# Kernel optimization log

Hardware: AMD Instinct MI355X
Metric: run time of the kernel (lower is better)

Reference implementation:

```python
import jax, jax.numpy as jnp
import numpy as np
import math

N_HEAD = 16
N_EMBD = 2048
HEAD_DIM = 128
N_LAYER = 24
EPS = 1e-5


def _get_alibi_slopes(n_heads):
    def pow2(n):
        start = 2 ** (-2 ** (-(math.log2(n) - 3)))
        return [start * start ** i for i in range(n)]
    if math.log2(n_heads).is_integer():
        return pow2(n_heads)
    c = 2 ** math.floor(math.log2(n_heads))
    s = pow2(c)
    extra = _get_alibi_slopes(2 * c)
    return s + extra[0::2][: n_heads - c]

ALIBI_SLOPES = jnp.asarray(np.array(_get_alibi_slopes(N_HEAD), dtype=np.float32))  # (H,)


def rmsnorm(x, w, eps=EPS):
    # fp32 RMSNorm over last dim with affine weight (use_fp32=True path)
    xf = x.astype(jnp.float32)
    out = xf * jax.lax.rsqrt(jnp.mean(xf * xf, axis=-1, keepdims=True) + eps)
    return (out * w.astype(jnp.float32)).astype(x.dtype)


def setup_inputs() -> dict:
    key = jax.random.key(0)
    ks = jax.random.split(key, 8)
    B, T, C, H, D = 2, 2048, N_EMBD, N_HEAD, HEAD_DIM
    sc = 1.0 / math.sqrt(C)
    proj_std = 0.5 / math.sqrt(C) / math.sqrt(N_LAYER)
    return {
        "x": jax.random.normal(ks[0], (B, T, C), jnp.float32),
        "Wq": jax.random.normal(ks[1], (C, H * D), jnp.float32) * sc,
        "Wk": jax.random.normal(ks[2], (C, H * D), jnp.float32) * sc,
        "Wv": jax.random.normal(ks[3], (C, H * D), jnp.float32) * sc,
        "Wproj": jax.random.normal(ks[4], (H * D, C), jnp.float32) * proj_std,
        "q_rms_w": jnp.ones((D,), jnp.float32),
        "k_rms_w": jnp.ones((D,), jnp.float32),
        "subln_w": jnp.ones((D,), jnp.float32),
    }


def reference(x, Wq, Wk, Wv, Wproj, q_rms_w, k_rms_w, subln_w):
    B, T, C = x.shape
    H, D = N_HEAD, HEAD_DIM
    q = (x @ Wq).reshape(B, T, H, D)
    k = (x @ Wk).reshape(B, T, H, D)
    v = (x @ Wv).reshape(B, T, H, D)
    # QK RMSNorm over head_dim
    q = rmsnorm(q, q_rms_w)
    k = rmsnorm(k, k_rms_w)
    # ALiBi bias: -slope * max(i-j, 0), plus causal mask
    idx = jnp.arange(T)
    dist = jnp.maximum(idx[:, None] - idx[None, :], 0).astype(jnp.float32)  # (T,T)
    bias = -dist[None, :, :] * ALIBI_SLOPES[:, None, None]  # (H,T,T)
    causal = idx[:, None] >= idx[None, :]  # (T,T)
    scale = 1.0 / math.sqrt(D)
    scores = jnp.einsum("bthd,bshd->bhts", q, k) * scale + bias[None]  # (B,H,T,T)
    scores = jnp.where(causal[None, None], scores, -jnp.inf)
    attn = jax.nn.softmax(scores, axis=-1)
    y = jnp.einsum("bhts,bshd->bhtd", attn, v)  # (B,H,T,D)
    y = rmsnorm(y, subln_w)  # post-attention groupnorm (subln)
    y = y.transpose(0, 2, 1, 3).reshape(B, T, H * D)
    return y @ Wproj
```

## Files before the change

kernel.cpp:

```cpp
#include <hip/hip_runtime.h>
#include <hip/hip_bf16.h>

#define Bc 2
#define Tc 2048
#define Cc 2048
#define Hc 16
#define Dc 128
#define BTc 4096
#define NQ 6144
#define EPSc 1e-5f
#define QSCALE 0.08838834764831845f

typedef __attribute__((ext_vector_type(8))) short bf16x8;
typedef __attribute__((ext_vector_type(4))) short bf16x4;
typedef __attribute__((ext_vector_type(4))) float f32x4;

typedef struct { unsigned short u[4]; } us4;

__device__ __forceinline__ f32x4 mfma16(bf16x8 a, bf16x8 b, f32x4 c) {
  return __builtin_amdgcn_mfma_f32_16x16x32_bf16(a, b, c, 0, 0, 0);
}

__device__ __forceinline__ void gload16(const void* g, void* l) {
  __builtin_amdgcn_global_load_lds(
      (const __attribute__((address_space(1))) void*)g,
      (__attribute__((address_space(3))) void*)l, 16, 0, 0);
}

__global__ __launch_bounds__(256) void k_xconv(const float* __restrict__ x,
                                               __hip_bfloat16* __restrict__ xb) {
  size_t i = ((size_t)blockIdx.x * 256 + threadIdx.x) * 4;
  float4 v = *(const float4*)(x + i);
  union { __hip_bfloat16 h[4]; bf16x4 v4; } u;
  u.h[0] = __float2bfloat16(v.x); u.h[1] = __float2bfloat16(v.y);
  u.h[2] = __float2bfloat16(v.z); u.h[3] = __float2bfloat16(v.w);
  *(bf16x4*)(xb + i) = u.v4;
}

__global__ __launch_bounds__(256) void k_wconv(const float* __restrict__ Wq,
    const float* __restrict__ Wk, const float* __restrict__ Wv,
    const float* __restrict__ Wp, __hip_bfloat16* __restrict__ Wqkv_t,
    __hip_bfloat16* __restrict__ Wproj_t) {
  __shared__ float tile[64][65];
  int z = blockIdx.z;
  const float* src = (z == 0) ? Wq : (z == 1) ? Wk : (z == 2) ? Wv : Wp;
  __hip_bfloat16* dst = (z < 3) ? (Wqkv_t + (size_t)z * Cc * Cc) : Wproj_t;
  int k0 = blockIdx.x * 64, n0 = blockIdx.y * 64;
  int l16 = threadIdx.x & 15, rg = threadIdx.x >> 4;
#pragma unroll
  for (int p = 0; p < 4; p++) {
    int r = p * 16 + rg;
    float4 v = *(const float4*)(src + (size_t)(k0 + r) * Cc + n0 + l16 * 4);
    tile[r][l16 * 4 + 0] = v.x; tile[r][l16 * 4 + 1] = v.y;
    tile[r][l16 * 4 + 2] = v.z; tile[r][l16 * 4 + 3] = v.w;
  }
  __syncthreads();
#pragma unroll
  for (int p = 0; p < 4; p++) {
    int rn = p * 16 + rg;
    int ck = l16 * 4;
    union { us4 s; unsigned long long q; } u;
#pragma unroll
    for (int j = 0; j < 4; j++) {
      union { __hip_bfloat16 h; unsigned short v; } cv;
      cv.h = __float2bfloat16(tile[ck + j][rn]);
      u.s.u[j] = cv.v;
    }
    *(unsigned long long*)(dst + (size_t)(n0 + rn) * Cc + k0 + ck) = u.q;
  }
}

__device__ __forceinline__ void mm48(f32x4 (&acc)[4][8], const bf16x8 (&A_)[4],
                                     const bf16x8 (&B_)[8]) {
  __builtin_amdgcn_s_setprio(1);
#pragma unroll
  for (int m = 0; m < 4; m++)
#pragma unroll
    for (int n = 0; n < 8; n++)
      acc[m][n] = mfma16(A_[m], B_[n], acc[m][n]);
  __builtin_amdgcn_s_setprio(0);
}

template <int MODE, typename OutT>
__global__ __launch_bounds__(256, 2) void k_gemm4(const __hip_bfloat16* __restrict__ A,
    const __hip_bfloat16* __restrict__ Bt, OutT* __restrict__ Co,
    int M, int N, const float* __restrict__ qw, const float* __restrict__ kw,
    __hip_bfloat16* __restrict__ Vt) {
  constexpr int K = 2048;
  __shared__ __align__(16) char lds[73728];
  const int nbx = M >> 7;
  const int nwg = nbx * (N >> 8);
  const int wg = blockIdx.x;
  const int swz = (wg & 7) * (nwg >> 3) + (wg >> 3);
  const int bx = swz % nbx, by = swz / nbx;
  const int tid = threadIdx.x, lane = tid & 63, wid = tid >> 6;
  const int wr = wid >> 1, wc = wid & 1;
  const int lr = lane & 15, lg = lane >> 4;
  const int xs = lg ^ ((lr >> 1) & 3);
  const int aoffR = (wr * 64 + lr) * 64 + xs * 16;
  const int boffR = 8192 + (wc * 128 + lr) * 64 + xs * 16;
  const int srow = lane >> 2;
  const int scolE = (((lane & 3) ^ ((lane >> 3) & 3)) << 3);
  const __hip_bfloat16* Ag = A + (size_t)(bx * 128 + wid * 32 + srow) * K + scolE;
  const __hip_bfloat16* Bg = Bt + (size_t)(by * 256 + wid * 64 + srow) * K + scolE;
  const size_t rK16 = (size_t)16 * K;
  char* dA = lds + wid * 2048;
  char* dB = lds + 8192 + wid * 4096;

#define STG(BUF, TS) {                                                   \
    gload16(Ag + (TS) * 32,        dA + (BUF) * 24576);                  \
    gload16(Ag + rK16 + (TS) * 32, dA + (BUF) * 24576 + 1024);           \
    gload16(Bg + (TS) * 32,            dB + (BUF) * 24576);              \
    gload16(Bg + rK16 + (TS) * 32,     dB + (BUF) * 24576 + 1024);       \
    gload16(Bg + 2 * rK16 + (TS) * 32, dB + (BUF) * 24576 + 2048);       \
    gload16(Bg + 3 * rK16 + (TS) * 32, dB + (BUF) * 24576 + 3072);       \
  }
#define BARRIER asm volatile("s_barrier" ::: "memory")
#define VW6 asm volatile("s_waitcnt vmcnt(6)" ::: "memory")
#define VW0 asm volatile("s_waitcnt vmcnt(0)" ::: "memory")

  f32x4 acc[4][8];
#pragma unroll
  for (int m = 0; m < 4; m++)
#pragma unroll
    for (int n = 0; n < 8; n++) acc[m][n] = f32x4{0.f, 0.f, 0.f, 0.f};
  bf16x8 rA[4], rB[8];

#define PH(RB, SB, TS, DOSTG, ENDW) {                                    \
    _Pragma("unroll")                                                    \
    for (int m = 0; m < 4; m++)                                          \
      rA[m] = *(const bf16x8*)(lds + (RB) * 24576 + aoffR + m * 1024);   \
    _Pragma("unroll")                                                    \
    for (int n = 0; n < 8; n++)                                          \
      rB[n] = *(const bf16x8*)(lds + (RB) * 24576 + boffR + n * 1024);   \
    if (DOSTG) STG((SB), (TS));                                          \
    mm48(acc, rA, rB);                                                   \
    ENDW;                                                                \
    BARRIER;                                                             \
  }

  STG(0, 0); STG(1, 1);
  VW6;
  BARRIER;

  for (int i = 0; i < 20; ++i) {
    const int t = 3 * i;
    PH(0, 2, t + 2, 1, VW6);
    PH(1, 0, t + 3, 1, VW6);
    PH(2, 1, t + 4, 1, VW6);
  }
  PH(0, 2, 62, 1, VW6);
  PH(1, 0, 63, 1, VW6);
  PH(2, 0, 0, 0, VW0);
  PH(0, 0, 0, 0, (void)0);
#undef PH
#undef STG
#undef BARRIER
#undef VW6
#undef VW0

  const int row0 = bx * 128 + wr * 64 + lg * 4;
  const int col0 = by * 256 + wc * 128 + lr;

  if (MODE == 1) {
    const int region = by >> 3;
    if (region < 2) {
      const float* wsel = (region == 0) ? qw : kw;
      const float extra = (region == 0) ? QSCALE : 1.0f;
      float wv[8];
#pragma unroll
      for (int n = 0; n < 8; n++) wv[n] = wsel[n * 16 + lr];
#pragma unroll
      for (int m = 0; m < 4; m++) {
        float ss[4] = {0.f, 0.f, 0.f, 0.f};
#pragma unroll
        for (int n = 0; n < 8; n++)
#pragma unroll
          for (int r = 0; r < 4; r++) ss[r] += acc[m][n][r] * acc[m][n][r];
        for (int msk = 1; msk < 16; msk <<= 1)
#pragma unroll
          for (int r = 0; r < 4; r++) ss[r] += __shfl_xor(ss[r], msk);
        float sc[4];
#pragma unroll
        for (int r = 0; r < 4; r++)
          sc[r] = rsqrtf(ss[r] * (1.0f / Dc) + EPSc) * extra;
#pragma unroll
        for (int n = 0; n < 8; n++) {
          size_t base = (size_t)(row0 + m * 16) * N + col0 + n * 16;
#pragma unroll
          for (int r = 0; r < 4; r++)
            ((__hip_bfloat16*)Co)[base + (size_t)r * N] =
                __float2bfloat16(acc[m][n][r] * sc[r] * wv[n]);
        }
      }
    } else {
      const int h = ((by - 16) * 256 + wc * 128) >> 7;
      const int bat = bx >> 4;
#pragma unroll
      for (int m = 0; m < 4; m++) {
        const int t0 = (row0 + m * 16) & (Tc - 1);
#pragma unroll
        for (int n = 0; n < 8; n++) {
          union { us4 p; unsigned long long q; } u;
#pragma unroll
          for (int r = 0; r < 4; r++) {
            union { __hip_bfloat16 h16; unsigned short s; } cv;
            cv.h16 = __float2bfloat16(acc[m][n][r]);
            u.p.u[r] = cv.s;
          }
          __hip_bfloat16* dst = Vt +
              ((size_t)(bat * 16 + h) * 128 + n * 16 + lr) * Tc + t0;
          *(unsigned long long*)dst = u.q;
        }
      }
    }
  } else {
#pragma unroll
    for (int m = 0; m < 4; m++)
#pragma unroll
      for (int n = 0; n < 8; n++) {
        size_t base = (size_t)(row0 + m * 16) * N + col0 + n * 16;
#pragma unroll
        for (int r = 0; r < 4; r++) {
          float v = acc[m][n][r];
          if constexpr (sizeof(OutT) == 2)
            Co[base + (size_t)r * N] = __float2bfloat16(v);
          else
            Co[base + (size_t)r * N] = v;
        }
      }
  }
}

__global__ __launch_bounds__(256, 2) void k_attn(const __hip_bfloat16* __restrict__ QKV,
    const __hip_bfloat16* __restrict__ Vt, const float* __restrict__ subw,
    __hip_bfloat16* __restrict__ Y) {
  __shared__ __align__(16) __hip_bfloat16 Ks[2][64][128];
  __shared__ __align__(16) __hip_bfloat16 Vs[2][128][64];
  __shared__ __align__(16) __hip_bfloat16 Plds[4][16][72];
  const int bh = blockIdx.x, pp = blockIdx.y;
  const int b = bh >> 4, h = bh & 15;
  const int w = threadIdx.x >> 6, lane = threadIdx.x & 63;
  const int lr = lane & 15, lg = lane >> 4;
  const float slope = exp2f(-0.5f * (float)(h + 1));
  const __hip_bfloat16* Kbase = QKV + (size_t)b * Tc * NQ + Cc + h * Dc;
  const __hip_bfloat16* Vbase = Vt + (size_t)bh * Dc * Tc;
  const int krow = (lane >> 4);
  const int kcolb = ((lane & 15) << 4);
  const int vrow = (lane >> 3);
  const int vcolb = ((lane & 7) << 4);
  f32x4 zero = {0.f, 0.f, 0.f, 0.f};

#define STAGE(bb, t)                                                              \
    {                                                                             \
      const int s0_ = (t) * 64;                                                   \
      for (int j = 0; j < 4; j++) {                                               \
        int row = w * 16 + j * 4 + krow;                                          \
        int cb = kcolb ^ ((row & 7) << 4);                                        \
        gload16(Kbase + (size_t)(s0_ + row) * NQ + (cb >> 1),                     \
                &Ks[bb][w * 16 + j * 4][0]);                                      \
      }                                                                           \
      for (int j = 0; j < 4; j++) {                                               \
        int row = w * 32 + j * 8 + vrow;                                          \
        int cb = vcolb ^ ((row & 7) << 4);                                        \
        gload16(Vbase + (size_t)row * Tc + s0_ + (cb >> 1),                       \
                &Vs[bb][w * 32 + j * 8][0]);                                      \
      }                                                                           \
    }
#define SBAR asm volatile("s_barrier" ::: "memory")
#define AVW8 asm volatile("s_waitcnt vmcnt(8)" ::: "memory")
#define AVW0 asm volatile("s_waitcnt vmcnt(0)" ::: "memory")
#define ALG0 asm volatile("s_waitcnt lgkmcnt(0)" ::: "memory")

  int buf = 0;
  for (int ti = 0; ti < 2; ti++) {
    const int qt = (ti == 0) ? (31 - pp) : pp;
    const int q0 = qt * 64 + w * 16;
    const int nchunk = qt + 1;
    bf16x8 aq[4];
    {
      const __hip_bfloat16* qb = QKV + (size_t)(b * Tc + q0 + lr) * NQ + h * Dc + lg * 8;
      for (int c = 0; c < 4; c++) aq[c] = *(const bf16x8*)(qb + c * 32);
    }
    f32x4 acc[8];
    for (int d = 0; d < 8; d++) acc[d] = zero;
    float mrow[4] = {-1e30f, -1e30f, -1e30f, -1e30f};
    float lsum[4] = {0.f, 0.f, 0.f, 0.f};

    SBAR;
    STAGE(buf, 0);
    for (int t = 0; t < nchunk; t++) {
      if (t + 1 < nchunk) { STAGE(buf ^ 1, t + 1); AVW8; }
      else                { AVW0; }
      SBAR;
      const int s0 = t * 64;
      f32x4 s[4];
      for (int ss = 0; ss < 4; ss++) s[ss] = zero;
      __builtin_amdgcn_s_setprio(1);
      for (int c = 0; c < 4; c++)
        for (int ss = 0; ss < 4; ss++) {
          int kr = ss * 16 + lr;
          const bf16x8 kf = *(const bf16x8*)
              &Ks[buf][kr][((c * 64 + lg * 16) ^ ((kr & 7) << 4)) >> 1];
          s[ss] = mfma16(aq[c], kf, s[ss]);
        }
      __builtin_amdgcn_s_setprio(0);
      const bool full = (s0 + 63 <= q0);
      float ps[4][4], mt[4];
      for (int r = 0; r < 4; r++) mt[r] = -1e30f;
      if (full) {
        for (int ss = 0; ss < 4; ss++) {
          int jj = s0 + ss * 16 + lr;
          for (int r = 0; r < 4; r++) {
            int i = q0 + lg * 4 + r;
            float pv = s[ss][r] - slope * (float)(i - jj);
            ps[ss][r] = pv;
            mt[r] = fmaxf(mt[r], pv);
          }
        }
      } else {
        for (int ss = 0; ss < 4; ss++) {
          int jj = s0 + ss * 16 + lr;
          for (int r = 0; r < 4; r++) {
            int i = q0 + lg * 4 + r;
            float pv = (jj <= i) ? s[ss][r] - slope * (float)(i - jj) : -1e30f;
            ps[ss][r] = pv;
            mt[r] = fmaxf(mt[r], pv);
          }
        }
      }
      for (int m = 1; m < 16; m <<= 1)
        for (int r = 0; r < 4; r++) mt[r] = fmaxf(mt[r], __shfl_xor(mt[r], m));
      float corr[4];
      for (int r = 0; r < 4; r++) {
        float mn = fmaxf(mrow[r], mt[r]);
        corr[r] = __expf(mrow[r] - mn);
        mrow[r] = mn;
      }
      for (int r = 0; r < 4; r++) lsum[r] *= corr[r];
      for (int ss = 0; ss < 4; ss++)
        for (int r = 0; r < 4; r++) {
          float e = __expf(ps[ss][r] - mrow[r]);
          ps[ss][r] = e;
          lsum[r] += e;
        }
      for (int d = 0; d < 8; d++)
        for (int r = 0; r < 4; r++) acc[d][r] *= corr[r];
      for (int ss = 0; ss < 4; ss++)
        for (int r = 0; r < 4; r++)
          Plds[w][lg * 4 + r][ss * 16 + lr] = __float2bfloat16(ps[ss][r]);
      bf16x8 pa0 = *(const bf16x8*)&Plds[w][lr][lg * 8];
      bf16x8 pa1 = *(const bf16x8*)&Plds[w][lr][32 + lg * 8];
      __builtin_amdgcn_s_setprio(1);
      for (int d = 0; d < 8; d++) {
        int vr = d * 16 + lr;
        const bf16x8 b0 = *(const bf16x8*)
            &Vs[buf][vr][((lg * 16) ^ ((vr & 7) << 4)) >> 1];
        const bf16x8 b1 = *(const bf16x8*)
            &Vs[buf][vr][((64 + lg * 16) ^ ((vr & 7) << 4)) >> 1];
        acc[d] = mfma16(pa0, b0, acc[d]);
        acc[d] = mfma16(pa1, b1, acc[d]);
      }
      __builtin_amdgcn_s_setprio(0);
      ALG0; SBAR;
      buf ^= 1;
    }
    for (int m = 1; m < 16; m <<= 1)
      for (int r = 0; r < 4; r++) lsum[r] += __shfl_xor(lsum[r], m);
    float ssum[4] = {0.f, 0.f, 0.f, 0.f};
    for (int r = 0; r < 4; r++) {
      float rl = 1.0f / lsum[r];
      for (int d = 0; d < 8; d++) {
        float o = acc[d][r] * rl;
        acc[d][r] = o;
        ssum[r] += o * o;
      }
    }
    for (int m = 1; m < 16; m <<= 1)
      for (int r = 0; r < 4; r++) ssum[r] += __shfl_xor(ssum[r], m);
    float ms[4];
    for (int r = 0; r < 4; r++) ms[r] = rsqrtf(ssum[r] * (1.0f / Dc) + EPSc);
    for (int d = 0; d < 8; d++) {
      float wv = subw[d * 16 + lr];
      for (int r = 0; r < 4; r++) {
        float y = acc[d][r] * ms[r] * wv;
        Y[(size_t)(b * Tc + q0 + lg * 4 + r) * Cc + h * Dc + d * 16 + lr] =
            __float2bfloat16(y);
      }
    }
  }
#undef STAGE
#undef SBAR
#undef AVW8
#undef AVW0
#undef ALG0
}

extern "C" void kernel_launch(void* const* d_in, const int* in_sizes, int n_in,
                              void* d_out, int out_size, void* d_ws, size_t ws_size,
                              hipStream_t stream) {
  const float* x  = (const float*)d_in[0];
  const float* Wq = (const float*)d_in[1];
  const float* Wk = (const float*)d_in[2];
  const float* Wv = (const float*)d_in[3];
  const float* Wp = (const float*)d_in[4];
  const float* qw = (const float*)d_in[5];
  const float* kw = (const float*)d_in[6];
  const float* sw = (const float*)d_in[7];
  float* out = (float*)d_out;

  char* ws = (char*)d_ws;
  __hip_bfloat16* Xb    = (__hip_bfloat16*)(ws + 0);
  __hip_bfloat16* Wqkv  = (__hip_bfloat16*)(ws + 16777216);
  __hip_bfloat16* Wproj = (__hip_bfloat16*)(ws + 41943040);
  __hip_bfloat16* QKV   = (__hip_bfloat16*)(ws + 50331648);
  __hip_bfloat16* Vt    = (__hip_bfloat16*)(ws + 100663296);
  __hip_bfloat16* Yb    = (__hip_bfloat16*)(ws + 117440512);

  k_xconv<<<dim3((BTc * Cc) / 1024), 256, 0, stream>>>(x, Xb);
  k_wconv<<<dim3(32, 32, 4), 256, 0, stream>>>(Wq, Wk, Wv, Wp, Wqkv, Wproj);
  k_gemm4<1, __hip_bfloat16><<<dim3((BTc / 128) * (NQ / 256)), 256, 0, stream>>>(
      Xb, Wqkv, QKV, BTc, NQ, qw, kw, Vt);
  k_attn<<<dim3(Bc * Hc, 16), 256, 0, stream>>>(QKV, Vt, sw, Yb);
  k_gemm4<0, float><<<dim3((BTc / 128) * (Cc / 256)), 256, 0, stream>>>(
      Yb, Wproj, out, BTc, Cc, nullptr, nullptr, nullptr);
}
```

Measured before the change: 252.4 us.

## Shrink GEMM tiles to 128x128 with 4 row-split waves for higher occupancy

Replaces the 128x256 GEMM tile, where waves are arranged 2x2, with a 128x128 tile in which each of the 4 waves owns 32 rows across the full 128 columns. LDS drops to 48KB and launch bounds rise to 3 blocks per CU. The grid doubles, giving better load balance across the CUs for the QKV and output projections. The cost is lower arithmetic intensity per tile, with more global and LDS B traffic per FLOP, and each wave rereads all of B from LDS.

```diff
diff --git a/kernel.cpp b/kernel.cpp
--- a/kernel.cpp
+++ b/kernel.cpp
@@ -70,11 +70,11 @@
   }
 }
 
-__device__ __forceinline__ void mm48(f32x4 (&acc)[4][8], const bf16x8 (&A_)[4],
+__device__ __forceinline__ void mm28(f32x4 (&acc)[2][8], const bf16x8 (&A_)[2],
                                      const bf16x8 (&B_)[8]) {
   __builtin_amdgcn_s_setprio(1);
 #pragma unroll
-  for (int m = 0; m < 4; m++)
+  for (int m = 0; m < 2; m++)
 #pragma unroll
     for (int n = 0; n < 8; n++)
       acc[m][n] = mfma16(A_[m], B_[n], acc[m][n]);
@@ -82,88 +82,86 @@
 }
 
 template <int MODE, typename OutT>
-__global__ __launch_bounds__(256, 2) void k_gemm4(const __hip_bfloat16* __restrict__ A,
+__global__ __launch_bounds__(256, 3) void k_gemmf(const __hip_bfloat16* __restrict__ A,
     const __hip_bfloat16* __restrict__ Bt, OutT* __restrict__ Co,
     int M, int N, const float* __restrict__ qw, const float* __restrict__ kw,
     __hip_bfloat16* __restrict__ Vt) {
   constexpr int K = 2048;
-  __shared__ __align__(16) char lds[73728];
+  __shared__ __align__(16) char lds[49152];
   const int nbx = M >> 7;
-  const int nwg = nbx * (N >> 8);
+  const int nwg = nbx * (N >> 7);
   const int wg = blockIdx.x;
   const int swz = (wg & 7) * (nwg >> 3) + (wg >> 3);
   const int bx = swz % nbx, by = swz / nbx;
   const int tid = threadIdx.x, lane = tid & 63, wid = tid >> 6;
-  const int wr = wid >> 1, wc = wid & 1;
   const int lr = lane & 15, lg = lane >> 4;
   const int xs = lg ^ ((lr >> 1) & 3);
-  const int aoffR = (wr * 64 + lr) * 64 + xs * 16;
-  const int boffR = 8192 + (wc * 128 + lr) * 64 + xs * 16;
-  const int srow = lane >> 2;
-  const int scolE = (((lane & 3) ^ ((lane >> 3) & 3)) << 3);
-  const __hip_bfloat16* Ag = A + (size_t)(bx * 128 + wid * 32 + srow) * K + scolE;
-  const __hip_bfloat16* Bg = Bt + (size_t)(by * 256 + wid * 64 + srow) * K + scolE;
-  const size_t rK16 = (size_t)16 * K;
-  char* dA = lds + wid * 2048;
-  char* dB = lds + 8192 + wid * 4096;
+  const int aoffR = (wid * 32 + lr) * 64 + xs * 16;
+  const int boffR = 8192 + lr * 64 + xs * 16;
+  const int srow = tid >> 2;
+  const int scolE = (((tid & 3) ^ ((tid >> 3) & 3)) << 3);
+  const __hip_bfloat16* Ag = A + (size_t)(bx * 128 + srow) * K + scolE;
+  const __hip_bfloat16* Bg = Bt + (size_t)(by * 128 + srow) * K + scolE;
+  const size_t r64K = (size_t)64 * K;
+  char* dA = lds + wid * 1024;
+  char* dB = lds + 8192 + wid * 1024;
 
 #define STG(BUF, TS) {                                                   \
-    gload16(Ag + (TS) * 32,        dA + (BUF) * 24576);                  \
-    gload16(Ag + rK16 + (TS) * 32, dA + (BUF) * 24576 + 1024);           \
-    gload16(Bg + (TS) * 32,            dB + (BUF) * 24576);              \
-    gload16(Bg + rK16 + (TS) * 32,     dB + (BUF) * 24576 + 1024);       \
-    gload16(Bg + 2 * rK16 + (TS) * 32, dB + (BUF) * 24576 + 2048);       \
-    gload16(Bg + 3 * rK16 + (TS) * 32, dB + (BUF) * 24576 + 3072);       \
+    gload16(Ag + (TS) * 32,        dA + (BUF));                          \
+    gload16(Ag + r64K + (TS) * 32, dA + (BUF) + 4096);                   \
+    gload16(Bg + (TS) * 32,        dB + (BUF));                          \
+    gload16(Bg + r64K + (TS) * 32, dB + (BUF) + 4096);                   \
   }
 #define BARRIER asm volatile("s_barrier" ::: "memory")
-#define VW6 asm volatile("s_waitcnt vmcnt(6)" ::: "memory")
+#define VW4 asm volatile("s_waitcnt vmcnt(4)" ::: "memory")
 #define VW0 asm volatile("s_waitcnt vmcnt(0)" ::: "memory")
 
-  f32x4 acc[4][8];
-#pragma unroll
-  for (int m = 0; m < 4; m++)
+  f32x4 acc[2][8];
+#pragma unroll
+  for (int m = 0; m < 2; m++)
 #pragma unroll
     for (int n = 0; n < 8; n++) acc[m][n] = f32x4{0.f, 0.f, 0.f, 0.f};
-  bf16x8 rA[4], rB[8];
+  bf16x8 rA[2], rB[8];
 
 #define PH(RB, SB, TS, DOSTG, ENDW) {                                    \
     _Pragma("unroll")                                                    \
-    for (int m = 0; m < 4; m++)                                          \
-      rA[m] = *(const bf16x8*)(lds + (RB) * 24576 + aoffR + m * 1024);   \
+    for (int m = 0; m < 2; m++)                                          \
+      rA[m] = *(const bf16x8*)(lds + (RB) * 16384 + aoffR + m * 1024);   \
     _Pragma("unroll")                                                    \
     for (int n = 0; n < 8; n++)                                          \
-      rB[n] = *(const bf16x8*)(lds + (RB) * 24576 + boffR + n * 1024);   \
-    if (DOSTG) STG((SB), (TS));                                          \
-    mm48(acc, rA, rB);                                                   \
+      rB[n] = *(const bf16x8*)(lds + (RB) * 16384 + boffR + n * 1024);   \
+    if (DOSTG) STG((SB) * 16384, (TS));                                  \
+    mm28(acc, rA, rB);                                                   \
     ENDW;                                                                \
     BARRIER;                                                             \
   }
 
-  STG(0, 0); STG(1, 1);
-  VW6;
+  STG(0, 0); STG(16384, 1);
+  VW4;
   BARRIER;
 
   for (int i = 0; i < 20; ++i) {
     const int t = 3 * i;
-    PH(0, 2, t + 2, 1, VW6);
-    PH(1, 0, t + 3, 1, VW6);
-    PH(2, 1, t + 4, 1, VW6);
-  }
-  PH(0, 2, 62, 1, VW6);
-  PH(1, 0, 63, 1, VW6);
+    PH(0, 2, t + 2, 1, VW4);
+    PH(1, 0, t + 3, 1, VW4);
+    PH(2, 1, t + 4, 1, VW4);
+  }
+  PH(0, 2, 62, 1, VW4);
+  PH(1, 0, 63, 1, VW4);
   PH(2, 0, 0, 0, VW0);
   PH(0, 0, 0, 0, (void)0);
 #undef PH
 #undef STG
 #undef BARRIER
-#undef VW6
+#undef VW4
 #undef VW0
 
-  const int row0 = bx * 128 + wr * 64 + lg * 4;
-  const int col0 = by * 256 + wc * 128 + lr;
+  const int row0 = bx * 128 + wid * 32 + lg * 4;
+  const int col0 = by * 128 + lr;
 
   if (MODE == 1) {
-    const int region = by >> 3;
+    const int region = by >> 4;
+    const int h = by & 15;
     if (region < 2) {
       const float* wsel = (region == 0) ? qw : kw;
       const float extra = (region == 0) ? QSCALE : 1.0f;
@@ -171,7 +169,7 @@
 #pragma unroll
       for (int n = 0; n < 8; n++) wv[n] = wsel[n * 16 + lr];
 #pragma unroll
-      for (int m = 0; m < 4; m++) {
+      for (int m = 0; m < 2; m++) {
         float ss[4] = {0.f, 0.f, 0.f, 0.f};
 #pragma unroll
         for (int n = 0; n < 8; n++)
@@ -194,10 +192,9 @@
         }
       }
     } else {
-      const int h = ((by - 16) * 256 + wc * 128) >> 7;
       const int bat = bx >> 4;
 #pragma unroll
-      for (int m = 0; m < 4; m++) {
+      for (int m = 0; m < 2; m++) {
         const int t0 = (row0 + m * 16) & (Tc - 1);
 #pragma unroll
         for (int n = 0; n < 8; n++) {
@@ -216,7 +213,7 @@
     }
   } else {
 #pragma unroll
-    for (int m = 0; m < 4; m++)
+    for (int m = 0; m < 2; m++)
 #pragma unroll
       for (int n = 0; n < 8; n++) {
         size_t base = (size_t)(row0 + m * 16) * N + col0 + n * 16;
@@ -419,9 +416,9 @@
 
   k_xconv<<<dim3((BTc * Cc) / 1024), 256, 0, stream>>>(x, Xb);
   k_wconv<<<dim3(32, 32, 4), 256, 0, stream>>>(Wq, Wk, Wv, Wp, Wqkv, Wproj);
-  k_gemm4<1, __hip_bfloat16><<<dim3((BTc / 128) * (NQ / 256)), 256, 0, stream>>>(
+  k_gemmf<1, __hip_bfloat16><<<dim3((BTc / 128) * (NQ / 128)), 256, 0, stream>>>(
       Xb, Wqkv, QKV, BTc, NQ, qw, kw, Vt);
   k_attn<<<dim3(Bc * Hc, 16), 256, 0, stream>>>(QKV, Vt, sw, Yb);
-  k_gemm4<0, float><<<dim3((BTc / 128) * (Cc / 256)), 256, 0, stream>>>(
+  k_gemmf<0, float><<<dim3((BTc / 128) * (Cc / 128)), 256, 0, stream>>>(
       Yb, Wproj, out, BTc, Cc, nullptr, nullptr, nullptr);
 }
```

After: 283.5 us. +12.3%, slower.
